# Kernel optimization log

Measured on AMD Instinct MI355X. Metric: run time of the kernel, lower is better.

## Reference

```python
import jax, jax.numpy as jnp
import numpy as np

N, D, F, O, R, G = 40000, 16, 128, 128, 4, 64  # nodes, max degree, in/out dim, relations, graphs


def setup_inputs() -> dict:
    key = jax.random.key(0)
    ks = jax.random.split(key, 16)
    s = 0.05
    feat = jax.random.normal(ks[0], (N, F), jnp.float32)
    nbrs = [jax.random.randint(ks[1 + i], (N, D), 0, N, jnp.int32) for i in range(4)]
    degs = [jax.random.randint(ks[5 + i], (N,), 0, D + 1, jnp.int32) for i in range(4)]
    seg_ids = jnp.sort(jax.random.randint(ks[9], (N,), 0, G, jnp.int32))
    lstm_Wih = jax.random.normal(ks[10], (R, 4 * F, F), jnp.float32) * s
    lstm_Whh = jax.random.normal(ks[11], (R, 4 * F, F), jnp.float32) * s
    lstm_b = jax.random.normal(ks[12], (R, 4 * F), jnp.float32) * s
    W_self = jax.random.normal(ks[13], (R, F, O), jnp.float32) * s
    W_neigh = jax.random.normal(ks[14], (R, F, O), jnp.float32) * s
    b_out = jax.random.normal(ks[15], (R, O), jnp.float32) * s
    return dict(feat=feat,
                nbr_intra_f=nbrs[0], deg_intra_f=degs[0],
                nbr_inter_f=nbrs[1], deg_inter_f=degs[1],
                nbr_intra_r=nbrs[2], deg_intra_r=degs[2],
                nbr_inter_r=nbrs[3], deg_inter_r=degs[3],
                seg_ids=seg_ids,
                lstm_Wih=lstm_Wih, lstm_Whh=lstm_Whh, lstm_b=lstm_b,
                W_self=W_self, W_neigh=W_neigh, b_out=b_out)


def _sage_lstm(feat, nbr, deg, Wih, Whh, b, Ws, Wn, bo):
    """SAGEConv with 'lstm' aggregator: gather padded neighbor features,
    run a masked LSTM over neighbor sequence, use final hidden state."""
    n, d = nbr.shape
    x = feat[nbr]                                   # [N, D, F] gathered neighbors
    mask = jnp.arange(d)[None, :] < deg[:, None]    # [N, D] valid-neighbor mask

    def step(carry, inp):
        h, c = carry
        xt, mt = inp                                # [N, F], [N]
        gates = xt @ Wih.T + h @ Whh.T + b          # [N, 4F]
        i, f, g, o = jnp.split(gates, 4, axis=-1)   # torch gate order: i, f, g, o
        i = jax.nn.sigmoid(i)
        f = jax.nn.sigmoid(f)
        g = jnp.tanh(g)
        o = jax.nn.sigmoid(o)
        cn = f * c + i * g
        hn = o * jnp.tanh(cn)
        m = mt[:, None]
        return (jnp.where(m, hn, h), jnp.where(m, cn, c)), None

    hdim = Whh.shape[1]
    init = (jnp.zeros((n, hdim), feat.dtype), jnp.zeros((n, hdim), feat.dtype))
    (h_fin, _), _ = jax.lax.scan(step, init, (jnp.swapaxes(x, 0, 1), mask.T))
    return feat @ Ws + h_fin @ Wn + bo              # fc_self + fc_neigh + bias


def reference(feat, nbr_intra_f, deg_intra_f, nbr_inter_f, deg_inter_f,
              nbr_intra_r, deg_intra_r, nbr_inter_r, deg_inter_r, seg_ids,
              lstm_Wih, lstm_Whh, lstm_b, W_self, W_neigh, b_out):
    # conv1 on forward graph, conv2 on reversed graph; HeteroGraphConv 'max' across relations
    def conv(r, nbr, deg):
        return _sage_lstm(feat, nbr, deg, lstm_Wih[r], lstm_Whh[r], lstm_b[r],
                          W_self[r], W_neigh[r], b_out[r])

    h1 = jnp.maximum(conv(0, nbr_intra_f, deg_intra_f), conv(1, nbr_inter_f, deg_inter_f))
    h2 = jnp.maximum(conv(2, nbr_intra_r, deg_intra_r), conv(3, nbr_inter_r, deg_inter_r))
    h = h1 + h2

    # per-graph mean of raw input features, broadcast back to nodes, then added
    ones = jnp.ones((feat.shape[0],), feat.dtype)
    cnt = jax.ops.segment_sum(ones, seg_ids, num_segments=G)
    sums = jax.ops.segment_sum(feat, seg_ids, num_segments=G)
    mean = sums / jnp.maximum(cnt, 1.0)[:, None]
    return mean[seg_ids] + h
```

## Files before the change

kernel.cpp:

```cpp
#include <hip/hip_runtime.h>
#include <hip/hip_bf16.h>

#define NN 40000
#define DDEG 16
#define FF 128
#define OO 128
#define NG 512
#define XIH_ELEMS 20480000
#define L2E 1.4426950408889634f
#define TWO_L2E 2.8853900817779268f

typedef short  s16x8 __attribute__((ext_vector_type(8)));
typedef unsigned short u16x8 __attribute__((ext_vector_type(8)));
typedef unsigned short u16x4 __attribute__((ext_vector_type(4)));
typedef float  f32x4 __attribute__((ext_vector_type(4)));

static_assert(sizeof(s16x8) == 16, "frag size");
static_assert(sizeof(__hip_bfloat16) == 2, "bf16 size");

__device__ __forceinline__ unsigned short f2bf(float f) {
    __hip_bfloat16 h = __float2bfloat16(f);
    return __builtin_bit_cast(unsigned short, h);
}
__device__ __forceinline__ float bf2f(unsigned short s) {
    unsigned int u = ((unsigned int)s) << 16;
    return __builtin_bit_cast(float, u);
}
__device__ __forceinline__ f32x4 splat4(float v) { f32x4 r = {v, v, v, v}; return r; }

__global__ void k_prep(const float* __restrict__ Wih, const float* __restrict__ Whh,
                       const float* __restrict__ Ws,  const float* __restrict__ Wn,
                       const float* __restrict__ feat,
                       unsigned short* __restrict__ wihb, unsigned short* __restrict__ whhb,
                       unsigned short* __restrict__ wstb, unsigned short* __restrict__ wntb,
                       unsigned short* __restrict__ fbf) {
    int i = blockIdx.x * blockDim.x + threadIdx.x;
    int stride = gridDim.x * blockDim.x;
    for (int idx = i; idx < 4 * NG * FF; idx += stride) {
        int row = (idx >> 7) & 511;
        float s = ((row >> 7) == 2) ? TWO_L2E : L2E;
        wihb[idx] = f2bf(Wih[idx] * s);
        whhb[idx] = f2bf(Whh[idx] * s);
    }
    for (int idx = i; idx < 4 * FF * OO; idx += stride) {
        int r = idx >> 14;
        int rem = idx & 16383;
        int o = rem >> 7;
        int k = rem & 127;
        wstb[idx] = f2bf(Ws[(r << 14) + (k << 7) + o]);
        wntb[idx] = f2bf(Wn[(r << 14) + (k << 7) + o]);
    }
    for (int idx4 = i * 4; idx4 < NN * FF; idx4 += stride * 4) {
        float4 v = *(const float4*)(feat + idx4);
        ushort4 o;
        o.x = f2bf(v.x); o.y = f2bf(v.y); o.z = f2bf(v.z); o.w = f2bf(v.w);
        *(ushort4*)(fbf + idx4) = o;
    }
}

__global__ void k_segmean(const float* __restrict__ feat, const int* __restrict__ seg,
                          float* __restrict__ mean) {
    int g = blockIdx.x;
    int lo, hi;
    { int a = 0, b = NN; while (a < b) { int m = (a + b) >> 1; if (seg[m] < g) a = m + 1; else b = m; } lo = a; }
    { int a = 0, b = NN; while (a < b) { int m = (a + b) >> 1; if (seg[m] < g + 1) a = m + 1; else b = m; } hi = a; }
    int tid = threadIdx.x;
    int d4 = tid & 31;
    int part = tid >> 5;
    float4 s = {0.f, 0.f, 0.f, 0.f};
    for (int row = lo + part; row < hi; row += 16) {
        float4 v = *(const float4*)(feat + (size_t)row * FF + d4 * 4);
        s.x += v.x; s.y += v.y; s.z += v.z; s.w += v.w;
    }
    __shared__ float ps[16][128];
    ps[part][d4 * 4 + 0] = s.x; ps[part][d4 * 4 + 1] = s.y;
    ps[part][d4 * 4 + 2] = s.z; ps[part][d4 * 4 + 3] = s.w;
    __syncthreads();
    if (tid < 128) {
        float tot = 0.f;
#pragma unroll
        for (int p = 0; p < 16; ++p) tot += ps[p][tid];
        mean[g * FF + tid] = tot / fmaxf((float)(hi - lo), 1.0f);
    }
}

__global__ void k_count(const int* __restrict__ D0, const int* __restrict__ D1,
                        const int* __restrict__ D2, const int* __restrict__ D3,
                        int* __restrict__ cnt4) {
    int r = blockIdx.y;
    const int* dg = (r == 0) ? D0 : (r == 1) ? D1 : (r == 2) ? D2 : D3;
    __shared__ int lcnt[17];
    if (threadIdx.x < 17) lcnt[threadIdx.x] = 0;
    __syncthreads();
    int n = blockIdx.x * blockDim.x + threadIdx.x;
    if (n < NN) { int d = dg[n]; if (d > 0) atomicAdd(&lcnt[d], 1); }
    __syncthreads();
    if (threadIdx.x >= 1 && threadIdx.x < 17 && lcnt[threadIdx.x])
        atomicAdd(&cnt4[r * 64 + threadIdx.x], lcnt[threadIdx.x]);
}
__global__ void k_offsets(int* __restrict__ cnt4) {
    int r = threadIdx.x;
    if (r < 4 && blockIdx.x == 0) {
        int running = 0;
        for (int d = 16; d >= 1; --d) {
            cnt4[r * 64 + 40 + d] = running;
            running += (cnt4[r * 64 + d] + 15) & ~15;
        }
    }
}
__global__ void k_scatter(const int* __restrict__ D0, const int* __restrict__ D1,
                          const int* __restrict__ D2, const int* __restrict__ D3,
                          int* __restrict__ cnt4, int* __restrict__ order4) {
    int r = blockIdx.y;
    const int* dg = (r == 0) ? D0 : (r == 1) ? D1 : (r == 2) ? D2 : D3;
    __shared__ int lcnt[17];
    __shared__ int gbase[17];
    if (threadIdx.x < 17) lcnt[threadIdx.x] = 0;
    __syncthreads();
    int n = blockIdx.x * blockDim.x + threadIdx.x;
    int d = 0, rank = 0;
    if (n < NN) { d = dg[n]; if (d > 0) rank = atomicAdd(&lcnt[d], 1); }
    __syncthreads();
    if (threadIdx.x >= 1 && threadIdx.x < 17 && lcnt[threadIdx.x])
        gbase[threadIdx.x] = atomicAdd(&cnt4[r * 64 + 40 + threadIdx.x], lcnt[threadIdx.x]);
    __syncthreads();
    if (n < NN && d > 0) order4[r * 40960 + gbase[d] + rank] = n;
}

__global__ __launch_bounds__(256, 4) void k_xih(const unsigned short* __restrict__ fbf,
                                                const unsigned short* __restrict__ wihb,
                                                const float* __restrict__ lb,
                                                unsigned short* __restrict__ xih, int rbase) {
    int r = rbase + blockIdx.y;
    unsigned short* xr = xih + (size_t)blockIdx.y * XIH_ELEMS;
    int tid = threadIdx.x;
    int w = tid >> 6;
    int l = tid & 63;
    int n0 = blockIdx.x * 32;
    int col = l & 15, grp = l >> 4;

    f32x4 acc[8][2];
#pragma unroll
    for (int j = 0; j < 8; ++j) {
        float sc = (((w + 4 * j) >> 3) == 2) ? TWO_L2E : L2E;
        f32x4 b = splat4(lb[r * NG + (w + 4 * j) * 16 + col] * sc);
        acc[j][0] = b; acc[j][1] = b;
    }

    s16x8 a0[4], a1[4];
    const unsigned short* ap0 = fbf + (size_t)(n0 + col) * FF + grp * 8;
    const unsigned short* ap1 = fbf + (size_t)(n0 + 16 + col) * FF + grp * 8;
#pragma unroll
    for (int kt = 0; kt < 4; ++kt) {
        a0[kt] = *(const s16x8*)(ap0 + kt * 32);
        a1[kt] = *(const s16x8*)(ap1 + kt * 32);
    }

    const unsigned short* wb = wihb + (size_t)r * NG * FF + col * FF + grp * 8;
#pragma unroll
    for (int j = 0; j < 8; ++j) {
#pragma unroll
        for (int kt = 0; kt < 4; ++kt) {
            s16x8 b = *(const s16x8*)(wb + (size_t)(w + 4 * j) * 16 * FF + kt * 32);
            acc[j][0] = __builtin_amdgcn_mfma_f32_16x16x32_bf16(a0[kt], b, acc[j][0], 0, 0, 0);
            acc[j][1] = __builtin_amdgcn_mfma_f32_16x16x32_bf16(a1[kt], b, acc[j][1], 0, 0, 0);
        }
    }
#pragma unroll
    for (int s = 0; s < 2; ++s) {
#pragma unroll
        for (int q = 0; q < 4; ++q) {
            int node = n0 + s * 16 + grp * 4 + q;
            u16x4 ue, uo;
#pragma unroll
            for (int m = 0; m < 4; ++m) {
                ue[m] = f2bf(acc[2 * m][s][q]);
                uo[m] = f2bf(acc[2 * m + 1][s][q]);
            }
            *(u16x4*)(xr + (size_t)node * NG + w * 64 + col * 4) = ue;
            *(u16x4*)(xr + (size_t)node * NG + (w + 4) * 64 + col * 4) = uo;
        }
    }
}

#define LSTM_BLOCKS 2560
__global__ __launch_bounds__(512, 4) void k_lstm(const unsigned short* __restrict__ xih,
                                                 const unsigned short* __restrict__ whhb,
                                                 const int* __restrict__ order4,
                                                 const int* __restrict__ N0, const int* __restrict__ N1,
                                                 const int* __restrict__ N2, const int* __restrict__ N3,
                                                 const int* __restrict__ D0, const int* __restrict__ D1,
                                                 const int* __restrict__ D2, const int* __restrict__ D3,
                                                 unsigned short* __restrict__ hfin4, int rbase) {
    int r = rbase + blockIdx.y;
    const unsigned short* xr = xih + (size_t)blockIdx.y * XIH_ELEMS;
    const int* nbr = (r == 0) ? N0 : (r == 1) ? N1 : (r == 2) ? N2 : N3;
    const int* deg = (r == 0) ? D0 : (r == 1) ? D1 : (r == 2) ? D2 : D3;
    const int* order = order4 + r * 40960;
    unsigned short* hfin = hfin4 + (size_t)r * NN * FF;

    __shared__ int nodes[16];
    __shared__ int nbrs_t[17][16];
    __shared__ unsigned short hbuf[2][2048];
    int tid = threadIdx.x;
    int w = tid >> 6, l = tid & 63;
    int col = l & 15, grp = l >> 4;

    int g0 = blockIdx.x * 16;
    if (tid < 16) nodes[tid] = order[g0 + tid];
    __syncthreads();
    if (nodes[0] < 0) return;
    int degv = deg[nodes[0]];

    const unsigned short* whhp = whhb + (size_t)r * NG * FF + col * FF + grp * 8;
    s16x8 breg[4][4];
#pragma unroll
    for (int j = 0; j < 4; ++j)
#pragma unroll
        for (int kt = 0; kt < 4; ++kt)
            breg[j][kt] = *(const s16x8*)(whhp + (size_t)(w + 8 * j) * 16 * FF + kt * 32);

    const char* xbc = (const char*)(xr + w * 64 + col * 4);

    int rbyte[4];
#pragma unroll
    for (int kt = 0; kt < 4; ++kt)
        rbyte[kt] = (col * 256 + kt * 64 + grp * 16) ^ ((col & 7) << 4);
    int wbyte[4];
#pragma unroll
    for (int q = 0; q < 4; ++q) {
        int node = grp * 4 + q;
        wbyte[q] = (node * 256 + (w * 16 + col) * 2) ^ ((node & 7) << 4);
    }

    if (tid < 256) {
        int row = tid >> 4, t = tid & 15;
        int nd = nodes[row]; if (nd < 0) nd = 0;
        nbrs_t[t][row] = nbr[nd * DDEG + t] << 10;
    }
    if (tid < 16) nbrs_t[16][tid] = 0;
    __syncthreads();

    f32x4 cst = splat4(0.f);

    u16x4 cur[4], nxt[4];
    {
        int4 of0 = *(const int4*)&nbrs_t[0][grp * 4];
        cur[0] = *(const u16x4*)(xbc + (unsigned)of0.x);
        cur[1] = *(const u16x4*)(xbc + (unsigned)of0.y);
        cur[2] = *(const u16x4*)(xbc + (unsigned)of0.z);
        cur[3] = *(const u16x4*)(xbc + (unsigned)of0.w);
    }

    for (int t = 0; t < degv; ++t) {
        {
            int4 ofn = *(const int4*)&nbrs_t[t + 1][grp * 4];
            nxt[0] = *(const u16x4*)(xbc + (unsigned)ofn.x);
            nxt[1] = *(const u16x4*)(xbc + (unsigned)ofn.y);
            nxt[2] = *(const u16x4*)(xbc + (unsigned)ofn.z);
            nxt[3] = *(const u16x4*)(xbc + (unsigned)ofn.w);
        }
        f32x4 acc[4];
#pragma unroll
        for (int j = 0; j < 4; ++j)
#pragma unroll
            for (int q = 0; q < 4; ++q)
                acc[j][q] = bf2f(cur[q][j]);

        if (t > 0) {
            const char* hrd = (const char*)hbuf[t & 1];
#pragma unroll
            for (int kt = 0; kt < 4; ++kt) {
                s16x8 ah = *(const s16x8*)(hrd + rbyte[kt]);
#pragma unroll
                for (int j = 0; j < 4; ++j)
                    acc[j] = __builtin_amdgcn_mfma_f32_16x16x32_bf16(ah, breg[j][kt], acc[j], 0, 0, 0);
            }
        }
        char* hwr = (char*)hbuf[(t + 1) & 1];
        {
            f32x4 Av, Bv, Cv, Dv;
#pragma unroll
            for (int q = 0; q < 4; ++q) {
                Av[q] = __builtin_amdgcn_exp2f(-acc[0][q]);
                Bv[q] = __builtin_amdgcn_exp2f(-acc[1][q]);
                Cv[q] = __builtin_amdgcn_exp2f(acc[2][q]);
                Dv[q] = __builtin_amdgcn_exp2f(-acc[3][q]);
            }
            f32x4 d1 = (Av + 1.0f) * (Cv + 1.0f);
            f32x4 d2 = Bv + 1.0f;
            f32x4 r1, r2;
#pragma unroll
            for (int q = 0; q < 4; ++q) {
                r1[q] = __builtin_amdgcn_rcpf(d1[q]);
                r2[q] = __builtin_amdgcn_rcpf(d2[q]);
            }
            f32x4 cv = cst * r2 + (Cv - 1.0f) * r1;
            cst = cv;
            f32x4 ecv = cv * TWO_L2E;
            f32x4 Ev;
#pragma unroll
            for (int q = 0; q < 4; ++q) Ev[q] = __builtin_amdgcn_exp2f(ecv[q]);
            f32x4 d3 = (Dv + 1.0f) * (Ev + 1.0f);
            f32x4 r3;
#pragma unroll
            for (int q = 0; q < 4; ++q) r3[q] = __builtin_amdgcn_rcpf(d3[q]);
            f32x4 hvv = (Ev - 1.0f) * r3;
#pragma unroll
            for (int q = 0; q < 4; ++q)
                *(unsigned short*)(hwr + wbyte[q]) = f2bf(hvv[q]);
        }
#pragma unroll
        for (int q = 0; q < 4; ++q) cur[q] = nxt[q];
        __syncthreads();
    }
    const char* hf = (const char*)hbuf[degv & 1];
    int row = tid >> 5;
    int nd = nodes[row];
    if (nd >= 0) {
        int off = (tid & 31) * 8;
        int byte = (row * 256 + off) ^ ((row & 7) << 4);
        u16x4 v = *(const u16x4*)(hf + byte);
        *(u16x4*)(hfin + (size_t)nd * FF + off / 2) = v;
    }
}

#define PROJ_BLOCKS_X 160
__global__ __launch_bounds__(256, 2) void k_projh(const unsigned short* __restrict__ fbf,
                                                  const unsigned short* __restrict__ hfin4,
                                                  const unsigned short* __restrict__ wstb,
                                                  const unsigned short* __restrict__ wntb,
                                                  const float* __restrict__ bo,
                                                  const int* __restrict__ D0, const int* __restrict__ D1,
                                                  const int* __restrict__ D2, const int* __restrict__ D3,
                                                  unsigned short* __restrict__ tmp) {
    int r = blockIdx.y >> 1;
    int half = blockIdx.y & 1;
    const int* dg = (r == 0) ? D0 : (r == 1) ? D1 : (r == 2) ? D2 : D3;
    int wv = threadIdx.x >> 6, l = threadIdx.x & 63;
    int col = l & 15, grp = l >> 4;

    const unsigned short* wsb = wstb + (size_t)r * OO * FF + col * FF + grp * 8;
    const unsigned short* wnb = wntb + (size_t)r * OO * FF + col * FF + grp * 8;
    s16x8 bws[4][4], bwn[4][4];
#pragma unroll
    for (int tt = 0; tt < 4; ++tt)
#pragma unroll
        for (int kt = 0; kt < 4; ++kt) {
            size_t toff = (size_t)((half * 4 + tt) * 16) * FF + kt * 32;
            bws[tt][kt] = *(const s16x8*)(wsb + toff);
            bwn[tt][kt] = *(const s16x8*)(wnb + toff);
        }
    float bias[4];
#pragma unroll
    for (int tt = 0; tt < 4; ++tt) bias[tt] = bo[r * OO + (half * 4 + tt) * 16 + col];

    const unsigned short* hbase = hfin4 + (size_t)r * NN * FF;
    unsigned short* tp = tmp + (size_t)r * NN * OO;
    const s16x8 zfrag = {0, 0, 0, 0, 0, 0, 0, 0};

    for (int c = blockIdx.x; c < 625; c += PROJ_BLOCKS_X) {
        int n0 = c * 64 + wv * 16;
        s16x8 af[4], ah[4];
        const unsigned short* fp = fbf + (size_t)(n0 + col) * FF + grp * 8;
        const unsigned short* hp = hbase + (size_t)(n0 + col) * FF + grp * 8;
        int dval = dg[n0 + col];
#pragma unroll
        for (int kt = 0; kt < 4; ++kt) {
            af[kt] = *(const s16x8*)(fp + kt * 32);
            s16x8 h = *(const s16x8*)(hp + kt * 32);
            ah[kt] = (dval > 0) ? h : zfrag;
        }
        f32x4 acc[4];
#pragma unroll
        for (int tt = 0; tt < 4; ++tt) acc[tt] = splat4(bias[tt]);
#pragma unroll
        for (int kt = 0; kt < 4; ++kt) {
#pragma unroll
            for (int tt = 0; tt < 4; ++tt) {
                acc[tt] = __builtin_amdgcn_mfma_f32_16x16x32_bf16(af[kt], bws[tt][kt], acc[tt], 0, 0, 0);
                acc[tt] = __builtin_amdgcn_mfma_f32_16x16x32_bf16(ah[kt], bwn[tt][kt], acc[tt], 0, 0, 0);
            }
        }
#pragma unroll
        for (int q = 0; q < 4; ++q) {
            int node = n0 + grp * 4 + q;
#pragma unroll
            for (int tt = 0; tt < 4; ++tt)
                tp[node * OO + (half * 4 + tt) * 16 + col] = f2bf(acc[tt][q]);
        }
    }
}

__global__ void k_combine(const unsigned short* __restrict__ tmp,
                          const float* __restrict__ mean, const int* __restrict__ seg,
                          float* __restrict__ out) {
    int i = blockIdx.x * blockDim.x + threadIdx.x;
    int idx4 = i * 4;
    if (idx4 >= NN * OO) return;
    int node = idx4 >> 7;
    int dim = idx4 & 127;
    ushort4 p0 = *(const ushort4*)(tmp + idx4);
    ushort4 p1 = *(const ushort4*)(tmp + (size_t)NN * OO + idx4);
    ushort4 p2 = *(const ushort4*)(tmp + 2 * (size_t)NN * OO + idx4);
    ushort4 p3 = *(const ushort4*)(tmp + 3 * (size_t)NN * OO + idx4);
    float4 mv = *(const float4*)(mean + seg[node] * FF + dim);
    float4 o;
    o.x = mv.x + fmaxf(bf2f(p0.x), bf2f(p1.x)) + fmaxf(bf2f(p2.x), bf2f(p3.x));
    o.y = mv.y + fmaxf(bf2f(p0.y), bf2f(p1.y)) + fmaxf(bf2f(p2.y), bf2f(p3.y));
    o.z = mv.z + fmaxf(bf2f(p0.z), bf2f(p1.z)) + fmaxf(bf2f(p2.z), bf2f(p3.z));
    o.w = mv.w + fmaxf(bf2f(p0.w), bf2f(p1.w)) + fmaxf(bf2f(p2.w), bf2f(p3.w));
    *(float4*)(out + idx4) = o;
}

extern "C" void kernel_launch(void* const* d_in, const int* in_sizes, int n_in,
                              void* d_out, int out_size, void* d_ws, size_t ws_size,
                              hipStream_t stream) {
    const float* feat = (const float*)d_in[0];
    const int* nbr[4] = {(const int*)d_in[1], (const int*)d_in[3], (const int*)d_in[5], (const int*)d_in[7]};
    const int* dgp[4] = {(const int*)d_in[2], (const int*)d_in[4], (const int*)d_in[6], (const int*)d_in[8]};
    const int* seg   = (const int*)d_in[9];
    const float* Wih = (const float*)d_in[10];
    const float* Whh = (const float*)d_in[11];
    const float* lb  = (const float*)d_in[12];
    const float* Ws  = (const float*)d_in[13];
    const float* Wn  = (const float*)d_in[14];
    const float* bo  = (const float*)d_in[15];

    char* ws = (char*)d_ws;
    float*          mean  = (float*)(ws + 0);
    unsigned short* fbf   = (unsigned short*)(ws + 32768);
    unsigned short* wihb  = (unsigned short*)(ws + 10272768);
    unsigned short* whhb  = (unsigned short*)(ws + 10797056);
    unsigned short* wstb  = (unsigned short*)(ws + 11321344);
    unsigned short* wntb  = (unsigned short*)(ws + 11452416);
    unsigned short* xih   = (unsigned short*)(ws + 11583488);

    const int big = (ws_size >= 217039872ULL);
    size_t xih_bytes = big ? 163840000ULL : 40960000ULL;
    unsigned short* hfin4 = (unsigned short*)(ws + 11583488 + xih_bytes);
    int*            order4= (int*)(ws + 11583488 + xih_bytes + 40960000);
    int*            cnt4  = (int*)(ws + 11583488 + xih_bytes + 40960000 + 655360);
    unsigned short* tmp   = xih;

    hipMemsetAsync(order4, 0xFF, 655360, stream);
    hipMemsetAsync(cnt4, 0, 1024, stream);

    k_prep<<<1024, 256, 0, stream>>>(Wih, Whh, Ws, Wn, feat, wihb, whhb, wstb, wntb, fbf);
    k_segmean<<<64, 512, 0, stream>>>(feat, seg, mean);
    k_count<<<dim3(157, 4), 256, 0, stream>>>(dgp[0], dgp[1], dgp[2], dgp[3], cnt4);
    k_offsets<<<1, 64, 0, stream>>>(cnt4);
    k_scatter<<<dim3(157, 4), 256, 0, stream>>>(dgp[0], dgp[1], dgp[2], dgp[3], cnt4, order4);

    if (big) {
        k_xih<<<dim3(1250, 4), 256, 0, stream>>>(fbf, wihb, lb, xih, 0);
        k_lstm<<<dim3(LSTM_BLOCKS, 4), 512, 0, stream>>>(xih, whhb, order4,
                                                         nbr[0], nbr[1], nbr[2], nbr[3],
                                                         dgp[0], dgp[1], dgp[2], dgp[3], hfin4, 0);
    } else {
        for (int r = 0; r < 4; ++r) {
            k_xih<<<dim3(1250, 1), 256, 0, stream>>>(fbf, wihb, lb, xih, r);
            k_lstm<<<dim3(LSTM_BLOCKS, 1), 512, 0, stream>>>(xih, whhb, order4,
                                                             nbr[0], nbr[1], nbr[2], nbr[3],
                                                             dgp[0], dgp[1], dgp[2], dgp[3], hfin4, r);
        }
    }
    k_projh<<<dim3(PROJ_BLOCKS_X, 8), 256, 0, stream>>>(fbf, hfin4, wstb, wntb, bo,
                                                        dgp[0], dgp[1], dgp[2], dgp[3], tmp);
    k_combine<<<5000, 256, 0, stream>>>(tmp, mean, seg, (float*)d_out);
}
```

Measured before the change: 514.9 us.

## Make xih and LSTM kernels persistent so weight fragments stay in registers

k_xih becomes a grid-stride persistent kernel with 128 blocks per relation. Each block loads the full Wih fragment set into registers once and then loops over 16-node chunks, instead of reloading weights for every 32-node tile. k_lstm now processes two 16-node groups per block, which halves the launch count and amortises the Whh register loads; it also drops the padded neighbour row by guarding the prefetch. The bf16 conversion is replaced by a manual round-to-nearest-even bit trick. The risks are fewer resident waves in k_xih, lower occupancy from the larger register footprint, and load imbalance across the persistent blocks.

```diff
diff --git a/kernel.cpp b/kernel.cpp
--- a/kernel.cpp
+++ b/kernel.cpp
@@ -1,5 +1,4 @@
 #include <hip/hip_runtime.h>
-#include <hip/hip_bf16.h>
 
 #define NN 40000
 #define DDEG 16
@@ -16,11 +15,11 @@
 typedef float  f32x4 __attribute__((ext_vector_type(4)));
 
 static_assert(sizeof(s16x8) == 16, "frag size");
-static_assert(sizeof(__hip_bfloat16) == 2, "bf16 size");
 
 __device__ __forceinline__ unsigned short f2bf(float f) {
-    __hip_bfloat16 h = __float2bfloat16(f);
-    return __builtin_bit_cast(unsigned short, h);
+    unsigned int u = __builtin_bit_cast(unsigned int, f);
+    u += 0x7FFFu + ((u >> 16) & 1u);
+    return (unsigned short)(u >> 16);
 }
 __device__ __forceinline__ float bf2f(unsigned short s) {
     unsigned int u = ((unsigned int)s) << 16;
@@ -127,7 +126,8 @@
     if (n < NN && d > 0) order4[r * 40960 + gbase[d] + rank] = n;
 }
 
-__global__ __launch_bounds__(256, 4) void k_xih(const unsigned short* __restrict__ fbf,
+#define XIH_BLOCKS_X 128
+__global__ __launch_bounds__(256, 2) void k_xih(const unsigned short* __restrict__ fbf,
                                                 const unsigned short* __restrict__ wihb,
                                                 const float* __restrict__ lb,
                                                 unsigned short* __restrict__ xih, int rbase) {
@@ -136,46 +136,47 @@
     int tid = threadIdx.x;
     int w = tid >> 6;
     int l = tid & 63;
-    int n0 = blockIdx.x * 32;
     int col = l & 15, grp = l >> 4;
 
-    f32x4 acc[8][2];
+    const unsigned short* wb = wihb + (size_t)r * NG * FF + col * FF + grp * 8;
+    s16x8 bx[8][4];
+#pragma unroll
+    for (int j = 0; j < 8; ++j)
+#pragma unroll
+        for (int kt = 0; kt < 4; ++kt)
+            bx[j][kt] = *(const s16x8*)(wb + (size_t)(w + 4 * j) * 16 * FF + kt * 32);
+
+    float bias[8];
 #pragma unroll
     for (int j = 0; j < 8; ++j) {
         float sc = (((w + 4 * j) >> 3) == 2) ? TWO_L2E : L2E;
-        f32x4 b = splat4(lb[r * NG + (w + 4 * j) * 16 + col] * sc);
-        acc[j][0] = b; acc[j][1] = b;
-    }
-
-    s16x8 a0[4], a1[4];
-    const unsigned short* ap0 = fbf + (size_t)(n0 + col) * FF + grp * 8;
-    const unsigned short* ap1 = fbf + (size_t)(n0 + 16 + col) * FF + grp * 8;
-#pragma unroll
-    for (int kt = 0; kt < 4; ++kt) {
-        a0[kt] = *(const s16x8*)(ap0 + kt * 32);
-        a1[kt] = *(const s16x8*)(ap1 + kt * 32);
-    }
-
-    const unsigned short* wb = wihb + (size_t)r * NG * FF + col * FF + grp * 8;
-#pragma unroll
-    for (int j = 0; j < 8; ++j) {
-#pragma unroll
-        for (int kt = 0; kt < 4; ++kt) {
-            s16x8 b = *(const s16x8*)(wb + (size_t)(w + 4 * j) * 16 * FF + kt * 32);
-            acc[j][0] = __builtin_amdgcn_mfma_f32_16x16x32_bf16(a0[kt], b, acc[j][0], 0, 0, 0);
-            acc[j][1] = __builtin_amdgcn_mfma_f32_16x16x32_bf16(a1[kt], b, acc[j][1], 0, 0, 0);
-        }
-    }
-#pragma unroll
-    for (int s = 0; s < 2; ++s) {
+        bias[j] = lb[r * NG + (w + 4 * j) * 16 + col] * sc;
+    }
+
+    for (int c = blockIdx.x; c < 2500; c += XIH_BLOCKS_X) {
+        int n0 = c * 16;
+        s16x8 a[4];
+        const unsigned short* ap = fbf + (size_t)(n0 + col) * FF + grp * 8;
+#pragma unroll
+        for (int kt = 0; kt < 4; ++kt) a[kt] = *(const s16x8*)(ap + kt * 32);
+
+        f32x4 acc[8];
+#pragma unroll
+        for (int j = 0; j < 8; ++j) acc[j] = splat4(bias[j]);
+#pragma unroll
+        for (int j = 0; j < 8; ++j)
+#pragma unroll
+            for (int kt = 0; kt < 4; ++kt)
+                acc[j] = __builtin_amdgcn_mfma_f32_16x16x32_bf16(a[kt], bx[j][kt], acc[j], 0, 0, 0);
+
 #pragma unroll
         for (int q = 0; q < 4; ++q) {
-            int node = n0 + s * 16 + grp * 4 + q;
+            int node = n0 + grp * 4 + q;
             u16x4 ue, uo;
 #pragma unroll
             for (int m = 0; m < 4; ++m) {
-                ue[m] = f2bf(acc[2 * m][s][q]);
-                uo[m] = f2bf(acc[2 * m + 1][s][q]);
+                ue[m] = f2bf(acc[2 * m][q]);
+                uo[m] = f2bf(acc[2 * m + 1][q]);
             }
             *(u16x4*)(xr + (size_t)node * NG + w * 64 + col * 4) = ue;
             *(u16x4*)(xr + (size_t)node * NG + (w + 4) * 64 + col * 4) = uo;
@@ -183,7 +184,8 @@
     }
 }
 
-#define LSTM_BLOCKS 2560
+#define LSTM_BLOCKS 1280
+#define LSTM_GROUPS 2
 __global__ __launch_bounds__(512, 4) void k_lstm(const unsigned short* __restrict__ xih,
                                                  const unsigned short* __restrict__ whhb,
                                                  const int* __restrict__ order4,
@@ -200,18 +202,12 @@
     unsigned short* hfin = hfin4 + (size_t)r * NN * FF;
 
     __shared__ int nodes[16];
-    __shared__ int nbrs_t[17][16];
+    __shared__ int nbrs_t[16][16];
     __shared__ unsigned short hbuf[2][2048];
     int tid = threadIdx.x;
     int w = tid >> 6, l = tid & 63;
     int col = l & 15, grp = l >> 4;
 
-    int g0 = blockIdx.x * 16;
-    if (tid < 16) nodes[tid] = order[g0 + tid];
-    __syncthreads();
-    if (nodes[0] < 0) return;
-    int degv = deg[nodes[0]];
-
     const unsigned short* whhp = whhb + (size_t)r * NG * FF + col * FF + grp * 8;
     s16x8 breg[4][4];
 #pragma unroll
@@ -233,95 +229,103 @@
         wbyte[q] = (node * 256 + (w * 16 + col) * 2) ^ ((node & 7) << 4);
     }
 
-    if (tid < 256) {
-        int row = tid >> 4, t = tid & 15;
-        int nd = nodes[row]; if (nd < 0) nd = 0;
-        nbrs_t[t][row] = nbr[nd * DDEG + t] << 10;
-    }
-    if (tid < 16) nbrs_t[16][tid] = 0;
-    __syncthreads();
-
-    f32x4 cst = splat4(0.f);
-
-    u16x4 cur[4], nxt[4];
-    {
-        int4 of0 = *(const int4*)&nbrs_t[0][grp * 4];
-        cur[0] = *(const u16x4*)(xbc + (unsigned)of0.x);
-        cur[1] = *(const u16x4*)(xbc + (unsigned)of0.y);
-        cur[2] = *(const u16x4*)(xbc + (unsigned)of0.z);
-        cur[3] = *(const u16x4*)(xbc + (unsigned)of0.w);
-    }
-
-    for (int t = 0; t < degv; ++t) {
+    for (int gi = 0; gi < LSTM_GROUPS; ++gi) {
+        int g0 = (blockIdx.x + gi * LSTM_BLOCKS) * 16;
+        __syncthreads();
+        if (tid < 16) nodes[tid] = order[g0 + tid];
+        __syncthreads();
+        if (nodes[0] < 0) continue;
+        int degv = deg[nodes[0]];
+
+        if (tid < 256) {
+            int row = tid >> 4, t = tid & 15;
+            int nd = nodes[row]; if (nd < 0) nd = 0;
+            nbrs_t[t][row] = nbr[nd * DDEG + t] << 10;
+        }
+        __syncthreads();
+
+        f32x4 cst = splat4(0.f);
+
+        u16x4 cur[4], nxt[4];
         {
-            int4 ofn = *(const int4*)&nbrs_t[t + 1][grp * 4];
-            nxt[0] = *(const u16x4*)(xbc + (unsigned)ofn.x);
-            nxt[1] = *(const u16x4*)(xbc + (unsigned)ofn.y);
-            nxt[2] = *(const u16x4*)(xbc + (unsigned)ofn.z);
-            nxt[3] = *(const u16x4*)(xbc + (unsigned)ofn.w);
-        }
-        f32x4 acc[4];
-#pragma unroll
-        for (int j = 0; j < 4; ++j)
-#pragma unroll
-            for (int q = 0; q < 4; ++q)
-                acc[j][q] = bf2f(cur[q][j]);
-
-        if (t > 0) {
-            const char* hrd = (const char*)hbuf[t & 1];
-#pragma unroll
-            for (int kt = 0; kt < 4; ++kt) {
-                s16x8 ah = *(const s16x8*)(hrd + rbyte[kt]);
-#pragma unroll
-                for (int j = 0; j < 4; ++j)
-                    acc[j] = __builtin_amdgcn_mfma_f32_16x16x32_bf16(ah, breg[j][kt], acc[j], 0, 0, 0);
+            int4 of0 = *(const int4*)&nbrs_t[0][grp * 4];
+            cur[0] = *(const u16x4*)(xbc + (unsigned)of0.x);
+            cur[1] = *(const u16x4*)(xbc + (unsigned)of0.y);
+            cur[2] = *(const u16x4*)(xbc + (unsigned)of0.z);
+            cur[3] = *(const u16x4*)(xbc + (unsigned)of0.w);
+        }
+
+        for (int t = 0; t < degv; ++t) {
+            if (t + 1 < degv) {
+                int4 ofn = *(const int4*)&nbrs_t[t + 1][grp * 4];
+                nxt[0] = *(const u16x4*)(xbc + (unsigned)ofn.x);
+                nxt[1] = *(const u16x4*)(xbc + (unsigned)ofn.y);
+                nxt[2] = *(const u16x4*)(xbc + (unsigned)ofn.z);
+                nxt[3] = *(const u16x4*)(xbc + (unsigned)ofn.w);
             }
-        }
-        char* hwr = (char*)hbuf[(t + 1) & 1];
-        {
-            f32x4 Av, Bv, Cv, Dv;
-#pragma unroll
-            for (int q = 0; q < 4; ++q) {
-                Av[q] = __builtin_amdgcn_exp2f(-acc[0][q]);
-                Bv[q] = __builtin_amdgcn_exp2f(-acc[1][q]);
-                Cv[q] = __builtin_amdgcn_exp2f(acc[2][q]);
-                Dv[q] = __builtin_amdgcn_exp2f(-acc[3][q]);
+            f32x4 acc[4];
+#pragma unroll
+            for (int j = 0; j < 4; ++j)
+#pragma unroll
+                for (int q = 0; q < 4; ++q)
+                    acc[j][q] = bf2f(cur[q][j]);
+
+            if (t > 0) {
+                const char* hrd = (const char*)hbuf[t & 1];
+#pragma unroll
+                for (int kt = 0; kt < 4; ++kt) {
+                    s16x8 ah = *(const s16x8*)(hrd + rbyte[kt]);
+#pragma unroll
+                    for (int j = 0; j < 4; ++j)
+                        acc[j] = __builtin_amdgcn_mfma_f32_16x16x32_bf16(ah, breg[j][kt], acc[j], 0, 0, 0);
+                }
             }
-            f32x4 d1 = (Av + 1.0f) * (Cv + 1.0f);
-            f32x4 d2 = Bv + 1.0f;
-            f32x4 r1, r2;
-#pragma unroll
-            for (int q = 0; q < 4; ++q) {
-                r1[q] = __builtin_amdgcn_rcpf(d1[q]);
-                r2[q] = __builtin_amdgcn_rcpf(d2[q]);
+            char* hwr = (char*)hbuf[(t + 1) & 1];
+            {
+                f32x4 Av, Bv, Cv, Dv;
+#pragma unroll
+                for (int q = 0; q < 4; ++q) {
+                    Av[q] = __builtin_amdgcn_exp2f(-acc[0][q]);
+                    Bv[q] = __builtin_amdgcn_exp2f(-acc[1][q]);
+                    Cv[q] = __builtin_amdgcn_exp2f(acc[2][q]);
+                    Dv[q] = __builtin_amdgcn_exp2f(-acc[3][q]);
+                }
+                f32x4 d1 = (Av + 1.0f) * (Cv + 1.0f);
+                f32x4 d2 = Bv + 1.0f;
+                f32x4 r1, r2;
+#pragma unroll
+                for (int q = 0; q < 4; ++q) {
+                    r1[q] = __builtin_amdgcn_rcpf(d1[q]);
+                    r2[q] = __builtin_amdgcn_rcpf(d2[q]);
+                }
+                f32x4 cv = cst * r2 + (Cv - 1.0f) * r1;
+                cst = cv;
+                f32x4 ecv = cv * TWO_L2E;
+                f32x4 Ev;
+#pragma unroll
+                for (int q = 0; q < 4; ++q) Ev[q] = __builtin_amdgcn_exp2f(ecv[q]);
+                f32x4 d3 = (Dv + 1.0f) * (Ev + 1.0f);
+                f32x4 r3;
+#pragma unroll
+                for (int q = 0; q < 4; ++q) r3[q] = __builtin_amdgcn_rcpf(d3[q]);
+                f32x4 hvv = (Ev - 1.0f) * r3;
+#pragma unroll
+                for (int q = 0; q < 4; ++q)
+                    *(unsigned short*)(hwr + wbyte[q]) = f2bf(hvv[q]);
             }
-            f32x4 cv = cst * r2 + (Cv - 1.0f) * r1;
-            cst = cv;
-            f32x4 ecv = cv * TWO_L2E;
-            f32x4 Ev;
-#pragma unroll
-            for (int q = 0; q < 4; ++q) Ev[q] = __builtin_amdgcn_exp2f(ecv[q]);
-            f32x4 d3 = (Dv + 1.0f) * (Ev + 1.0f);
-            f32x4 r3;
-#pragma unroll
-            for (int q = 0; q < 4; ++q) r3[q] = __builtin_amdgcn_rcpf(d3[q]);
-            f32x4 hvv = (Ev - 1.0f) * r3;
-#pragma unroll
-            for (int q = 0; q < 4; ++q)
-                *(unsigned short*)(hwr + wbyte[q]) = f2bf(hvv[q]);
-        }
-#pragma unroll
-        for (int q = 0; q < 4; ++q) cur[q] = nxt[q];
-        __syncthreads();
-    }
-    const char* hf = (const char*)hbuf[degv & 1];
-    int row = tid >> 5;
-    int nd = nodes[row];
-    if (nd >= 0) {
-        int off = (tid & 31) * 8;
-        int byte = (row * 256 + off) ^ ((row & 7) << 4);
-        u16x4 v = *(const u16x4*)(hf + byte);
-        *(u16x4*)(hfin + (size_t)nd * FF + off / 2) = v;
+#pragma unroll
+            for (int q = 0; q < 4; ++q) cur[q] = nxt[q];
+            __syncthreads();
+        }
+        const char* hf = (const char*)hbuf[degv & 1];
+        int row = tid >> 5;
+        int nd = nodes[row];
+        if (nd >= 0) {
+            int off = (tid & 31) * 8;
+            int byte = (row * 256 + off) ^ ((row & 7) << 4);
+            u16x4 v = *(const u16x4*)(hf + byte);
+            *(u16x4*)(hfin + (size_t)nd * FF + off / 2) = v;
+        }
     }
 }
 
@@ -453,13 +457,13 @@
     k_scatter<<<dim3(157, 4), 256, 0, stream>>>(dgp[0], dgp[1], dgp[2], dgp[3], cnt4, order4);
 
     if (big) {
-        k_xih<<<dim3(1250, 4), 256, 0, stream>>>(fbf, wihb, lb, xih, 0);
+        k_xih<<<dim3(XIH_BLOCKS_X, 4), 256, 0, stream>>>(fbf, wihb, lb, xih, 0);
         k_lstm<<<dim3(LSTM_BLOCKS, 4), 512, 0, stream>>>(xih, whhb, order4,
                                                          nbr[0], nbr[1], nbr[2], nbr[3],
                                                          dgp[0], dgp[1], dgp[2], dgp[3], hfin4, 0);
     } else {
         for (int r = 0; r < 4; ++r) {
-            k_xih<<<dim3(1250, 1), 256, 0, stream>>>(fbf, wihb, lb, xih, r);
+            k_xih<<<dim3(XIH_BLOCKS_X, 1), 256, 0, stream>>>(fbf, wihb, lb, xih, r);
             k_lstm<<<dim3(LSTM_BLOCKS, 1), 512, 0, stream>>>(xih, whhb, order4,
                                                              nbr[0], nbr[1], nbr[2], nbr[3],
                                                              dgp[0], dgp[1], dgp[2], dgp[3], hfin4, r);
```

New measurement: 426.8 us. 1.21x faster.
